# Performance work log

Hardware: AMD Instinct MI355X
Metric: run time of the kernel (lower is better)

Reference implementation:

```python
import jax, jax.numpy as jnp
import numpy as np

N_FEAT = 1024
N_LAYER = 4  # n_layer + 1 in the original module


def setup_inputs() -> dict:
    key = jax.random.key(0)
    kx, kw, kb = jax.random.split(key, 3)
    x = jax.random.normal(kx, (16384, N_FEAT), dtype=jnp.float32)
    weight_w = jax.random.normal(kw, (N_LAYER, N_FEAT), dtype=jnp.float32)
    weight_b = jax.random.normal(kb, (N_LAYER, N_FEAT), dtype=jnp.float32)
    return {"x": x, "weight_w": weight_w, "weight_b": weight_b}


def reference(x, weight_w, weight_b):
    # Original per layer: x_{i+1} = x0 @ x_i^T @ w_i + b_i + x_i  (per sample).
    # (x0 x_i^T) w = x0 * <x_i, w>, so we use the O(n) equivalent form and
    # never materialize the [B, n, n] outer product.
    x0 = x  # [B, n]
    xi = x0
    for i in range(N_LAYER):
        xiw = jnp.einsum("bn,n->b", xi, weight_w[i])  # [B]
        xi = x0 * xiw[:, None] + weight_b[i][None, :] + xi
    return xi
```

## Files before the change

kernel.cpp:

```cpp
#include <hip/hip_runtime.h>

#define N_FEAT 1024
#define N_LAYER 4
#define RPG 8
#define GPB 4
#define AS1 __attribute__((address_space(1)))
#define AS3 __attribute__((address_space(3)))

__global__ __launch_bounds__(256) void crossnet_kernel(
    const float* __restrict__ x,
    const float* __restrict__ weight_w,
    const float* __restrict__ weight_b,
    float* __restrict__ out,
    int n_rows) {
  const int wave = threadIdx.x >> 6;
  const int lane = threadIdx.x & 63;

  __shared__ float buf[2][RPG * N_FEAT];

  float4 w[4][N_LAYER];
  float4 csum[4];
  float e[N_LAYER] = {0.f, 0.f, 0.f, 0.f};
#pragma unroll
  for (int c = 0; c < 4; ++c) {
#pragma unroll
    for (int i = 0; i < N_LAYER; ++i)
      w[c][i] = ((const float4*)(weight_w + i * N_FEAT))[c * 64 + lane];
    float4 cum = make_float4(0.f, 0.f, 0.f, 0.f);
#pragma unroll
    for (int i = 0; i < N_LAYER; ++i) {
      if (i > 0)
        e[i] += cum.x * w[c][i].x + cum.y * w[c][i].y +
                cum.z * w[c][i].z + cum.w * w[c][i].w;
      const float4 b = ((const float4*)(weight_b + i * N_FEAT))[c * 64 + lane];
      cum.x += b.x; cum.y += b.y; cum.z += b.z; cum.w += b.w;
    }
    csum[c] = cum;
  }
#pragma unroll
  for (int off = 32; off > 0; off >>= 1)
#pragma unroll
    for (int i = 1; i < N_LAYER; ++i) e[i] += __shfl_xor(e[i], off, 64);

  const int row0 = blockIdx.x * (RPG * GPB);
  if (row0 >= n_rows) return;

  auto stage = [&](int bsel, int grow) {
#pragma unroll
    for (int j = 0; j < 8; ++j) {
      const float* gsrc = x + (size_t)(grow + 2 * wave + (j >> 2)) * N_FEAT +
                          ((j & 3) * 64 + lane) * 4;
      float* ldst = &buf[bsel][(wave * 2 + (j >> 2)) * N_FEAT + (j & 3) * 256];
      __builtin_amdgcn_global_load_lds((const AS1 unsigned int*)gsrc,
                                       (AS3 unsigned int*)ldst, 16, 0, 0);
    }
  };

  stage(0, row0);

#pragma unroll
  for (int t = 0; t < GPB; ++t) {
    const int grow = row0 + t * RPG;

    __builtin_amdgcn_sched_barrier(0);
    if (t + 1 < GPB) stage((t + 1) & 1, grow + RPG);

    if (t == 0 || t == GPB - 1) {
      asm volatile("s_waitcnt vmcnt(8)" ::: "memory");
    } else {
      asm volatile("s_waitcnt vmcnt(16)" ::: "memory");
    }
    __builtin_amdgcn_sched_barrier(0);

    const float* B = buf[t & 1];

    float4 xv[2][4];
    float p[2 * N_LAYER];
#pragma unroll
    for (int k = 0; k < 2 * N_LAYER; ++k) p[k] = 0.f;
#pragma unroll
    for (int r = 0; r < 2; ++r) {
#pragma unroll
      for (int c = 0; c < 4; ++c) {
        xv[r][c] = *(const float4*)&B[(wave * 2 + r) * N_FEAT +
                                      (c * 64 + lane) * 4];
#pragma unroll
        for (int i = 0; i < N_LAYER; ++i) {
          p[r * N_LAYER + i] += xv[r][c].x * w[c][i].x + xv[r][c].y * w[c][i].y +
                                xv[r][c].z * w[c][i].z + xv[r][c].w * w[c][i].w;
        }
      }
    }

#pragma unroll
    for (int off = 32; off > 0; off >>= 1)
#pragma unroll
      for (int k = 0; k < 2 * N_LAYER; ++k) p[k] += __shfl_xor(p[k], off, 64);

#pragma unroll
    for (int r = 0; r < 2; ++r) {
      float A = 1.f;
#pragma unroll
      for (int i = 0; i < N_LAYER; ++i)
        A += A * p[r * N_LAYER + i] + e[i];
      const size_t row = grow + wave * 2 + r;
#pragma unroll
      for (int c = 0; c < 4; ++c) {
        float4 o;
        o.x = fmaf(xv[r][c].x, A, csum[c].x);
        o.y = fmaf(xv[r][c].y, A, csum[c].y);
        o.z = fmaf(xv[r][c].z, A, csum[c].z);
        o.w = fmaf(xv[r][c].w, A, csum[c].w);
        ((float4*)out)[row * 256 + c * 64 + lane] = o;
      }
    }
  }
}

extern "C" void kernel_launch(void* const* d_in, const int* in_sizes, int n_in,
                              void* d_out, int out_size, void* d_ws, size_t ws_size,
                              hipStream_t stream) {
  const float* x = (const float*)d_in[0];
  const float* ww = (const float*)d_in[1];
  const float* wb = (const float*)d_in[2];
  float* out = (float*)d_out;

  const int n_rows = in_sizes[0] / N_FEAT;
  const int rows_per_block = RPG * GPB;
  const int n_blocks = (n_rows + rows_per_block - 1) / rows_per_block;
  crossnet_kernel<<<n_blocks, 256, 0, stream>>>(x, ww, wb, out, n_rows);
}
```

Before: 116.8 us.

## Process one row per wave per stage and move bias cumsum to LDS

Halves the rows staged per group from 8 to 4, so each wave handles one row per step instead of two. The per-lane bias cumulative sums move from registers into a small shared-memory table. Launch bounds now request 4 blocks per CU. Together these cut register and LDS use per block to raise occupancy, which should help latency hiding on this memory-bound kernel. The cost is twice as many blocks, each with less in-flight data, plus an extra LDS read per output chunk.

```diff
diff --git a/kernel.cpp b/kernel.cpp
--- a/kernel.cpp
+++ b/kernel.cpp
@@ -2,12 +2,12 @@
 
 #define N_FEAT 1024
 #define N_LAYER 4
-#define RPG 8
+#define RPG 4
 #define GPB 4
 #define AS1 __attribute__((address_space(1)))
 #define AS3 __attribute__((address_space(3)))
 
-__global__ __launch_bounds__(256) void crossnet_kernel(
+__global__ __launch_bounds__(256, 4) void crossnet_kernel(
     const float* __restrict__ x,
     const float* __restrict__ weight_w,
     const float* __restrict__ weight_b,
@@ -17,9 +17,9 @@
   const int lane = threadIdx.x & 63;
 
   __shared__ float buf[2][RPG * N_FEAT];
+  __shared__ float4 csum_lds[4 * 64];
 
   float4 w[4][N_LAYER];
-  float4 csum[4];
   float e[N_LAYER] = {0.f, 0.f, 0.f, 0.f};
 #pragma unroll
   for (int c = 0; c < 4; ++c) {
@@ -35,7 +35,7 @@
       const float4 b = ((const float4*)(weight_b + i * N_FEAT))[c * 64 + lane];
       cum.x += b.x; cum.y += b.y; cum.z += b.z; cum.w += b.w;
     }
-    csum[c] = cum;
+    csum_lds[c * 64 + lane] = cum;
   }
 #pragma unroll
   for (int off = 32; off > 0; off >>= 1)
@@ -47,10 +47,10 @@
 
   auto stage = [&](int bsel, int grow) {
 #pragma unroll
-    for (int j = 0; j < 8; ++j) {
-      const float* gsrc = x + (size_t)(grow + 2 * wave + (j >> 2)) * N_FEAT +
-                          ((j & 3) * 64 + lane) * 4;
-      float* ldst = &buf[bsel][(wave * 2 + (j >> 2)) * N_FEAT + (j & 3) * 256];
+    for (int c = 0; c < 4; ++c) {
+      const float* gsrc =
+          x + (size_t)(grow + wave) * N_FEAT + (c * 64 + lane) * 4;
+      float* ldst = &buf[bsel][wave * N_FEAT + c * 256];
       __builtin_amdgcn_global_load_lds((const AS1 unsigned int*)gsrc,
                                        (AS3 unsigned int*)ldst, 16, 0, 0);
     }
@@ -66,53 +66,44 @@
     if (t + 1 < GPB) stage((t + 1) & 1, grow + RPG);
 
     if (t == 0 || t == GPB - 1) {
+      asm volatile("s_waitcnt vmcnt(4)" ::: "memory");
+    } else {
       asm volatile("s_waitcnt vmcnt(8)" ::: "memory");
-    } else {
-      asm volatile("s_waitcnt vmcnt(16)" ::: "memory");
     }
     __builtin_amdgcn_sched_barrier(0);
 
     const float* B = buf[t & 1];
 
-    float4 xv[2][4];
-    float p[2 * N_LAYER];
+    float4 xv[4];
+    float p[N_LAYER] = {0.f, 0.f, 0.f, 0.f};
 #pragma unroll
-    for (int k = 0; k < 2 * N_LAYER; ++k) p[k] = 0.f;
+    for (int c = 0; c < 4; ++c) {
+      xv[c] = *(const float4*)&B[wave * N_FEAT + (c * 64 + lane) * 4];
 #pragma unroll
-    for (int r = 0; r < 2; ++r) {
-#pragma unroll
-      for (int c = 0; c < 4; ++c) {
-        xv[r][c] = *(const float4*)&B[(wave * 2 + r) * N_FEAT +
-                                      (c * 64 + lane) * 4];
-#pragma unroll
-        for (int i = 0; i < N_LAYER; ++i) {
-          p[r * N_LAYER + i] += xv[r][c].x * w[c][i].x + xv[r][c].y * w[c][i].y +
-                                xv[r][c].z * w[c][i].z + xv[r][c].w * w[c][i].w;
-        }
-      }
+      for (int i = 0; i < N_LAYER; ++i)
+        p[i] += xv[c].x * w[c][i].x + xv[c].y * w[c][i].y +
+                xv[c].z * w[c][i].z + xv[c].w * w[c][i].w;
     }
 
 #pragma unroll
     for (int off = 32; off > 0; off >>= 1)
 #pragma unroll
-      for (int k = 0; k < 2 * N_LAYER; ++k) p[k] += __shfl_xor(p[k], off, 64);
+      for (int i = 0; i < N_LAYER; ++i) p[i] += __shfl_xor(p[i], off, 64);
 
+    float A = 1.f;
 #pragma unroll
-    for (int r = 0; r < 2; ++r) {
-      float A = 1.f;
+    for (int i = 0; i < N_LAYER; ++i) A += A * p[i] + e[i];
+
+    const size_t row = grow + wave;
 #pragma unroll
-      for (int i = 0; i < N_LAYER; ++i)
-        A += A * p[r * N_LAYER + i] + e[i];
-      const size_t row = grow + wave * 2 + r;
-#pragma unroll
-      for (int c = 0; c < 4; ++c) {
-        float4 o;
-        o.x = fmaf(xv[r][c].x, A, csum[c].x);
-        o.y = fmaf(xv[r][c].y, A, csum[c].y);
-        o.z = fmaf(xv[r][c].z, A, csum[c].z);
-        o.w = fmaf(xv[r][c].w, A, csum[c].w);
-        ((float4*)out)[row * 256 + c * 64 + lane] = o;
-      }
+    for (int c = 0; c < 4; ++c) {
+      const float4 cs = csum_lds[c * 64 + lane];
+      float4 o;
+      o.x = fmaf(xv[c].x, A, cs.x);
+      o.y = fmaf(xv[c].y, A, cs.y);
+      o.z = fmaf(xv[c].z, A, cs.z);
+      o.w = fmaf(xv[c].w, A, cs.w);
+      ((float4*)out)[row * 256 + c * 64 + lane] = o;
     }
   }
 }
```

Measured after the change: 125.3 us. 7.3% more time.
